# Performance work log

Measured on AMD Instinct MI355X. Metric: run time of the kernel, lower is better.

## Reference

```python
import jax, jax.numpy as jnp
import numpy as np

N, U, K, S = 1024, 64, 2, 2        # nodes, rnn_units, max_diffusion_step, num_supports
Q = S * K + 1                       # diffusion matrices (incl. identity)
B, T, H = 64, 12, 12                # batch, seq_len, horizon
IN, OUT, L = 1, 1, 2                # input_dim, output_dim, num_rnn_layers


def setup_inputs() -> dict:
    key = jax.random.key(0)
    ks = jax.random.split(key, 16)

    def glorot(k, shape):
        fan = shape[0] + shape[-1]
        return jax.random.normal(k, shape, jnp.float32) * np.float32(np.sqrt(2.0 / fan))

    # random-walk supports from a random dense adjacency (DCRNN: transpose of D^-1 A)
    adj = jax.random.uniform(ks[0], (N, N), jnp.float32)
    rw = lambda a: a / a.sum(axis=1, keepdims=True)
    supports = jnp.stack([rw(adj).T, rw(adj.T).T])  # (S, N, N)

    inputs = jax.random.normal(ks[1], (B, N * IN, T), jnp.float32)

    p = {}
    i = 2
    for pre, ind in (("enc", IN), ("dec", OUT)):
        for l in range(L):
            f = (ind if l == 0 else U) + U
            p[f"{pre}_gw{l}"] = glorot(ks[i], (Q * f, 2 * U)); i += 1
            p[f"{pre}_gb{l}"] = jnp.ones((2 * U,), jnp.float32)   # GRU gate bias init 1.0
            p[f"{pre}_cw{l}"] = glorot(ks[i], (Q * f, U)); i += 1
            p[f"{pre}_cb{l}"] = jnp.zeros((U,), jnp.float32)
    p["proj_w"] = glorot(ks[i], (U, OUT))
    p["proj_b"] = jnp.zeros((OUT,), jnp.float32)
    return {"inputs": inputs, "supports": supports, **p}


def _diffusion(x, supports):
    # x: (B, N, F) -> (B, N, Q*F); Chebyshev-style recurrence as in DCGRUCell._gconv
    mats = [x]
    for s in range(S):
        A = supports[s]
        x0 = x
        x1 = jnp.einsum('nm,bmf->bnf', A, x0)
        mats.append(x1)
        for _ in range(2, K + 1):
            x2 = 2.0 * jnp.einsum('nm,bmf->bnf', A, x1) - x0
            mats.append(x2)
            x0, x1 = x1, x2
    return jnp.concatenate(mats, axis=-1)


def _cell(x, h, supports, gw, gb, cw, cb):
    # x: (B,N,Fin), h: (B,N,U)
    ru = jax.nn.sigmoid(_diffusion(jnp.concatenate([x, h], -1), supports) @ gw + gb)
    r, u = ru[..., :U], ru[..., U:]
    c = jnp.tanh(_diffusion(jnp.concatenate([x, r * h], -1), supports) @ cw + cb)
    return u * h + (1.0 - u) * c


def reference(inputs, supports,
              enc_gw0, enc_gb0, enc_cw0, enc_cb0,
              enc_gw1, enc_gb1, enc_cw1, enc_cb1,
              dec_gw0, dec_gb0, dec_cw0, dec_cb0,
              dec_gw1, dec_gb1, dec_cw1, dec_cb1,
              proj_w, proj_b):
    enc = [(enc_gw0, enc_gb0, enc_cw0, enc_cb0), (enc_gw1, enc_gb1, enc_cw1, enc_cb1)]
    dec = [(dec_gw0, dec_gb0, dec_cw0, dec_cb0), (dec_gw1, dec_gb1, dec_cw1, dec_cb1)]

    x_seq = inputs.reshape(B, N, IN, T).transpose(3, 0, 1, 2)  # (T, B, N, IN)
    h0 = jnp.zeros((L, B, N, U), inputs.dtype)

    def enc_step(h, x):
        out, hs = x, []
        for l in range(L):
            hn = _cell(out, h[l], supports, *enc[l])
            hs.append(hn)
            out = hn
        return jnp.stack(hs), None

    hT, _ = jax.lax.scan(enc_step, h0, x_seq)

    def dec_step(carry, _):
        h, xin = carry
        out, hs = xin, []
        for l in range(L):
            hn = _cell(out, h[l], supports, *dec[l])
            hs.append(hn)
            out = hn
        proj = out @ proj_w + proj_b          # (B, N, OUT)
        return (jnp.stack(hs), proj), proj.reshape(B, N * OUT)

    go = jnp.zeros((B, N, OUT), inputs.dtype)
    _, outs = jax.lax.scan(dec_step, (hT, go), None, length=H)
    return outs  # (H, B, N*OUT)
```

## Files before the change

### kernel.cpp

```cpp
#include <hip/hip_runtime.h>

typedef _Float16 f16;
typedef _Float16 f16x4 __attribute__((ext_vector_type(4)));
typedef _Float16 f16x8 __attribute__((ext_vector_type(8)));
typedef float    f32x4 __attribute__((ext_vector_type(4)));

#define NN 1024
#define NT 12
#define NHOR 12
#define ROWS (NN*64)
#define MATH (1024*1024)
static const long SLOT = (long)NN*4096;

__device__ __forceinline__ int sw4(int row){ return (row ^ (row>>2)) & 3; }

__device__ __forceinline__ int ilvpos(int k){
  int r = k & 31;
  return (k & ~31) + ((r & 12) << 1) + (r & 3) + ((r & 16) >> 2);
}

template<int NR>
__device__ __forceinline__ void stage(f16* lds, const f16* src, int ldk, int k0, int tid){
  #pragma unroll
  for (int ic=0; ic<NR/64; ++ic){
    const int c = tid + ic*256;
    const int row = c>>2, c4 = c&3;
    const f16* g = src + (long)row*ldk + k0 + ((c4 ^ sw4(row))<<3);
    __builtin_amdgcn_global_load_lds((const __attribute__((address_space(1))) void*)g,
                                     (__attribute__((address_space(3))) void*)(lds + c*8), 16, 0, 0);
  }
}

__device__ __forceinline__ f16x8 fragI(const f16* lds, int row, int rq){
  return *(const f16x8*)&lds[row*32 + ((rq ^ sw4(row))<<3)];
}

__device__ __forceinline__ f16x8 fragN(const f16* lds, int row, int lk){
  const int s = sw4(row);
  const int cl = (lk>>3) ^ s, ch = (2|(lk>>3)) ^ s;
  f16x4 lo = *(const f16x4*)&lds[row*32 + (cl<<3) + (lk&7)];
  f16x4 hi = *(const f16x4*)&lds[row*32 + (ch<<3) + (lk&7)];
  f16x8 r; r[0]=lo[0];r[1]=lo[1];r[2]=lo[2];r[3]=lo[3];
  r[4]=hi[0];r[5]=hi[1];r[6]=hi[2];r[7]=hi[3];
  return r;
}

struct DiffP {
  const f16* W;
  const f16* Y0; const f16* Y1;
  f16* out0; f16* out1;
  int nct0;
  int mode_x;
  int wsq;
};

__global__ __launch_bounds__(256) void gemm_diff(DiffP p) {
  __shared__ f16 Ws[2][128*32];
  __shared__ f16 Ys[2][128*32];
  const int tid=threadIdx.x, l=tid&63, w=tid>>6;
  const int rq=l>>4, ro=l&15, lk=rq*4;
  const int rt=blockIdx.x, ct=blockIdx.y;
  const int part = (ct >= p.nct0);
  const int ctl  = part ? (ct - p.nct0) : ct;
  const f16* Wb = p.W + (long)rt*128*1024;
  const f16* Yb = (part ? p.Y1 : p.Y0) + (long)ctl*128*1024;
  const int wm=(w>>1)*64, wc=(w&1)*64;
  f32x4 acc[4][4] = {};
  stage<128>(Ws[0], Wb, 1024, 0, tid);
  stage<128>(Ys[0], Yb, 1024, 0, tid);
  __syncthreads();
  int cur = 0;
  for (int t=0; t<32; ++t) {
    if (t<31) {
      stage<128>(Ws[cur^1], Wb, 1024, (t+1)*32, tid);
      stage<128>(Ys[cur^1], Yb, 1024, (t+1)*32, tid);
    }
    f16x8 wf[4], yf[4];
    #pragma unroll
    for (int i=0;i<4;i++) wf[i] = fragI(Ws[cur], wm + i*16 + ro, rq);
    #pragma unroll
    for (int j=0;j<4;j++) yf[j] = fragI(Ys[cur], wc + j*16 + ro, rq);
    if (!p.wsq) {
      #pragma unroll
      for (int i=0;i<4;i++)
        #pragma unroll
        for (int j=0;j<4;j++)
          acc[i][j] = __builtin_amdgcn_mfma_f32_16x16x32_f16(wf[i], yf[j], acc[i][j], 0,0,0);
    } else {
      #pragma unroll
      for (int i=0;i<4;i++)
        #pragma unroll
        for (int j=0;j<4;j++)
          acc[i][j] = __builtin_amdgcn_mfma_f32_16x16x32_f16(yf[j], wf[i], acc[i][j], 0,0,0);
    }
    __syncthreads();
    cur ^= 1;
  }
  if (p.wsq) {
    #pragma unroll
    for (int i=0;i<4;i++){
      const long rg = (long)rt*128 + wm + i*16 + ro;
      #pragma unroll
      for (int j=0;j<4;j++){
        const int cb = ct*128 + wc + j*16 + lk;
        f16x4 sv;
        #pragma unroll
        for (int e=0;e<4;e++) sv[e] = (f16)(2.f*acc[i][j][e] - ((rg==(long)(cb+e))?1.f:0.f));
        *(f16x4*)&p.out0[rg*1024 + cb] = sv;
      }
    }
    return;
  }
  f16* ob = part ? p.out1 : p.out0;
  const int mode = part ? p.mode_x : 0;
  #pragma unroll
  for (int i=0;i<4;i++){
    #pragma unroll
    for (int e=0;e<4;e++){
      const int c = rt*128 + wm + i*16 + rq*4 + e;
      const int q = c>>10, n = c&1023;
      #pragma unroll
      for (int j=0;j<4;j++){
        const int bul = wc + j*16 + ro;
        const f16 v = (f16)acc[i][j][e];
        if (mode==0) ob[(long)q*SLOT + (long)n*4096 + (long)ctl*128 + bul] = v;
        else if (bul < 64) ob[(long)q*ROWS + n*64 + bul] = v;
      }
    }
  }
}

struct Tab5 { const f16* p[5]; };
struct CellP {
  Tab5 ta, tb, xq;
  const f16 *wa, *wb, *wx0;
  const float* bias;
  const float* h32in;
  f16* rh; f16* rhhat; float* u32;
  float* h32io; f16* h16io; f16* hhat;
  int nseg, xf1;
};

template<int O, int GATE>
__global__ __launch_bounds__(256) void cell_gemm(CellP p) {
  constexpr int FC = O/32;
  __shared__ f16 As[2][128*32];
  __shared__ f16 Bs[2][O*32];
  const int tid=threadIdx.x, l=tid&63, w=tid>>6;
  const int rq=l>>4, ro=l&15, lk=rq*4;
  const int wm=(w>>1)*64, wc=(w&1)*(O/2);
  f32x4 acc[4][FC] = {};
  const long r0 = (long)blockIdx.x*128;
  const int nt = p.nseg*10;
  auto stg = [&](int buf, int t){
    const int kg = t*32;
    const int seg = (kg>=320)?1:0;
    const int kk = kg - seg*320;
    const int q = kk>>6, kq = kk&63;
    const f16* asrc = (seg ? p.tb.p[q] : p.ta.p[q]) + r0*64;
    const f16* wsrc = seg ? p.wb : p.wa;
    stage<128>(As[buf], asrc, 64, kq, tid);
    stage<O>(Bs[buf], wsrc, 320, kk, tid);
  };
  stg(0,0);
  __syncthreads();
  int cur = 0;
  for (int t=0; t<nt; ++t) {
    if (t+1<nt) stg(cur^1, t+1);
    f16x8 a[4], b[FC];
    #pragma unroll
    for (int i=0;i<4;i++) a[i] = fragN(As[cur], wm + i*16 + ro, lk);
    #pragma unroll
    for (int j=0;j<FC;j++) b[j] = fragI(Bs[cur], wc + j*16 + ro, rq);
    #pragma unroll
    for (int i=0;i<4;i++)
      #pragma unroll
      for (int j=0;j<FC;j++)
        acc[i][j] = __builtin_amdgcn_mfma_f32_16x16x32_f16(a[i], b[j], acc[i][j], 0,0,0);
    __syncthreads();
    cur ^= 1;
  }
  #pragma unroll
  for (int i=0;i<4;i++) {
    #pragma unroll
    for (int e=0;e<4;e++) {
      const long rg = r0 + wm + i*16 + rq*4 + e;
      const int bb = (int)(rg & 63), nn2 = (int)(rg >> 6);
      const long hcol = (long)ilvpos(nn2);
      float xv[5];
      if (p.xf1) {
        #pragma unroll
        for (int q2=0;q2<5;q2++) xv[q2] = (float)p.xq.p[q2][rg];
      }
      #pragma unroll
      for (int j=0;j<FC;j++) {
        const int col = wc + j*16 + ro;
        float v = acc[i][j][e] + p.bias[col];
        if (p.xf1) {
          #pragma unroll
          for (int q2=0;q2<5;q2++) v += xv[q2] * (float)p.wx0[q2*O + col];
        }
        if (GATE) {
          const float s = 1.f/(1.f + __expf(-v));
          if (col < 64) {
            const float rhv = s * p.h32in[rg*64 + col];
            p.rh[rg*64 + col] = (f16)rhv;
            p.rhhat[((long)bb*64 + col)*1024 + hcol] = (f16)rhv;
          } else {
            p.u32[rg*64 + (col-64)] = s;
          }
        } else {
          const float cc = tanhf(v);
          const float u  = p.u32[rg*64 + col];
          const float h  = p.h32io[rg*64 + col];
          const float hn = u*h + (1.f-u)*cc;
          p.h32io[rg*64 + col] = hn;
          p.h16io[rg*64 + col] = (f16)hn;
          p.hhat[((long)bb*64 + col)*1024 + hcol] = (f16)hn;
        }
      }
    }
  }
}

__global__ __launch_bounds__(256) void k_transpose(const f16* in, f16* out, int R, int C) {
  __shared__ f16 T[64*66];
  const long rb = (long)blockIdx.x*64, cb = (long)blockIdx.y*64;
  const int t = threadIdx.x;
  #pragma unroll
  for (int it=0; it<2; ++it) {
    const int r = (t>>3) + it*32, c8 = (t&7)*8;
    f16x8 v = *(const f16x8*)(in + (rb+r)*C + cb + c8);
    *(f16x8*)&T[r*66 + c8] = v;
  }
  __syncthreads();
  #pragma unroll
  for (int it=0; it<2; ++it) {
    const int c = (t>>3) + it*32, r8 = (t&7)*8;
    f16x8 v;
    #pragma unroll
    for (int j=0;j<8;j++) v[j] = T[(r8+j)*66 + c];
    *(f16x8*)(out + (cb+c)*R + rb + r8) = v;
  }
}

__global__ void k_cast_sup(const float* s, f16* o) {
  long i = (long)blockIdx.x*256 + threadIdx.x;
  if (i < 2LL*MATH) o[i] = (f16)s[i];
}

__global__ void k_ilv(const f16* in, f16* out) {
  int i = blockIdx.x*256 + threadIdx.x;
  if (i >= MATH) return;
  int r = i>>10, k = i&1023;
  out[(long)r*1024 + ilvpos(k)] = in[i];
}

__global__ void k_pack_x(const float* in, f16* xe, f16* xet) {
  int i = blockIdx.x*256 + threadIdx.x;
  if (i >= NT*ROWS) return;
  int t = i / ROWS, r = i % ROWS, n = r>>6, b = r&63;
  float v = in[(long)b*NN*NT + (long)n*NT + t];
  xe[i] = (f16)v;
  xet[(long)t*131072 + (long)b*1024 + ilvpos(n)] = (f16)v;
}

__global__ void k_split_w_t(const float* src, f16* wh_t, f16* wxA, int f, int xf, int O) {
  int i = blockIdx.x*256 + threadIdx.x;
  if (i >= 5*f*O) return;
  int o = i % O, rr = i / O, q = rr / f, ff = rr % f;
  f16 v = (f16)src[i];
  if (ff < xf) {
    if (xf == 1) wxA[q*O + o] = v;
    else         wxA[(long)o*320 + q*64 + ilvpos(ff)] = v;
  } else {
    wh_t[(long)o*320 + q*64 + ilvpos(ff - xf)] = v;
  }
}

__global__ void k_proj(const float* h32, const float* pw, const float* pb,
                       float* out, f16* xdec, f16* xdect) {
  int r = blockIdx.x*256 + threadIdx.x;
  if (r >= ROWS) return;
  float acc = pb[0];
  const float* hp = h32 + (long)r*64;
  #pragma unroll
  for (int k=0;k<64;k++) acc += hp[k]*pw[k];
  int n = r>>6, b = r&63;
  out[(long)b*NN + n] = acc;
  xdec[r] = (f16)acc;
  xdect[(long)b*1024 + ilvpos(n)] = (f16)acc;
}

extern "C" void kernel_launch(void* const* d_in, const int* in_sizes, int n_in,
                              void* d_out, int out_size, void* d_ws, size_t ws_size,
                              hipStream_t stream) {
  (void)in_sizes; (void)n_in; (void)out_size; (void)ws_size;
  const float* inputs = (const float*)d_in[0];
  const float* sup    = (const float*)d_in[1];
  const float* gwp[4] = {(const float*)d_in[2], (const float*)d_in[6], (const float*)d_in[10], (const float*)d_in[14]};
  const float* gbp[4] = {(const float*)d_in[3], (const float*)d_in[7], (const float*)d_in[11], (const float*)d_in[15]};
  const float* cwp[4] = {(const float*)d_in[4], (const float*)d_in[8], (const float*)d_in[12], (const float*)d_in[16]};
  const float* cbp[4] = {(const float*)d_in[5], (const float*)d_in[9], (const float*)d_in[13], (const float*)d_in[17]};
  const float* pw = (const float*)d_in[18];
  const float* pb = (const float*)d_in[19];
  float* out = (float*)d_out;

  char* base = (char*)d_ws; size_t off = 0;
  auto alloc = [&](size_t bytes)->void* { void* p = base + off; off += (bytes + 255) & ~(size_t)255; return p; };
  f16* W16int = (f16*)alloc(4LL*MATH*2);
  f16* xenc   = (f16*)alloc((long)NT*ROWS*2);
  f16* xet    = (f16*)alloc((long)NT*131072*2);
  f16* xdec   = (f16*)alloc((long)ROWS*2);
  f16* xdect  = (f16*)alloc(131072L*2);
  f16*  h16[2]  = {(f16*)alloc((long)ROWS*64*2),  (f16*)alloc((long)ROWS*64*2)};
  f16*  hh[2]   = {(f16*)alloc(4096L*1024*2),     (f16*)alloc(4096L*1024*2)};
  float* h32[2] = {(float*)alloc((long)ROWS*64*4), (float*)alloc((long)ROWS*64*4)};
  float* u32 = (float*)alloc((long)ROWS*64*4);
  f16* rh    = (f16*)alloc((long)ROWS*64*2);
  f16* rhh   = (f16*)alloc(4096L*1024*2);
  f16* Dh    = (f16*)alloc(4*SLOT*2);
  f16* Dx    = (f16*)alloc(4*SLOT*2);
  f16* Dx0   = (f16*)alloc(4LL*ROWS*2);
  f16 *gwh[4], *gwx[4], *cwh[4], *cwx[4];
  for (int i=0;i<4;i++) {
    gwh[i]=(f16*)alloc(128L*320*2); gwx[i]=(f16*)alloc(128L*320*2);
    cwh[i]=(f16*)alloc(64L*320*2);  cwx[i]=(f16*)alloc(64L*320*2);
  }

  hipMemsetAsync(h16[0], 0, (long)ROWS*64*2, stream);
  hipMemsetAsync(h16[1], 0, (long)ROWS*64*2, stream);
  hipMemsetAsync(hh[0],  0, 4096L*1024*2, stream);
  hipMemsetAsync(hh[1],  0, 4096L*1024*2, stream);
  hipMemsetAsync(h32[0], 0, (long)ROWS*64*4, stream);
  hipMemsetAsync(h32[1], 0, (long)ROWS*64*4, stream);
  hipMemsetAsync(xdec,   0, (long)ROWS*2, stream);
  hipMemsetAsync(xdect,  0, 131072L*2, stream);

  f16* tmpA   = Dh;
  f16* tmpAt  = Dh + 2L*MATH;
  f16* tmpAti = Dh + 4L*MATH;
  f16* tmpSq  = Dh + 5L*MATH;
  k_cast_sup<<<(2*MATH+255)/256, 256, 0, stream>>>(sup, tmpA);
  for (int s=0;s<2;s++) {
    k_transpose<<<dim3(16,16),256,0,stream>>>(tmpA + (long)s*MATH, tmpAt + (long)s*MATH, 1024, 1024);
    k_ilv<<<4096,256,0,stream>>>(tmpA + (long)s*MATH, W16int + (long)(2*s)*MATH);
  }
  for (int s=0;s<2;s++) {
    k_ilv<<<4096,256,0,stream>>>(tmpAt + (long)s*MATH, tmpAti);
    DiffP mp{};
    mp.W = W16int + (long)(2*s)*MATH; mp.Y0 = tmpAti; mp.Y1 = tmpAti;
    mp.out0 = tmpSq; mp.nct0 = 8; mp.wsq = 1;
    gemm_diff<<<dim3(8,8),256,0,stream>>>(mp);
    k_ilv<<<4096,256,0,stream>>>(tmpSq, W16int + (long)(2*s+1)*MATH);
  }
  k_pack_x<<<(NT*ROWS+255)/256,256,0,stream>>>(inputs, xenc, xet);
  const int fs[4]  = {65,128,65,128};
  const int xfs[4] = {1,64,1,64};
  for (int i=0;i<4;i++) {
    k_split_w_t<<<(5*fs[i]*128+255)/256,256,0,stream>>>(gwp[i], gwh[i], gwx[i], fs[i], xfs[i], 128);
    k_split_w_t<<<(5*fs[i]*64 +255)/256,256,0,stream>>>(cwp[i], cwh[i], cwx[i], fs[i], xfs[i], 64);
  }

  auto run_cell = [&](const f16* xraw, const f16* xhat, int xf,
                      f16* h16c, f16* hhatc, float* h32c, int wi) {
    DiffP dp{};
    dp.W = W16int; dp.Y0 = hhatc; dp.out0 = Dh; dp.nct0 = 32; dp.wsq = 0;
    int gy;
    if (xf == 64) { dp.Y1 = xhat; dp.out1 = Dx;  dp.mode_x = 0; gy = 64; }
    else          { dp.Y1 = xhat; dp.out1 = Dx0; dp.mode_x = 2; gy = 33; }
    gemm_diff<<<dim3(32, gy), 256, 0, stream>>>(dp);
    CellP gp{};
    gp.ta.p[0] = h16c; for (int q=1;q<5;q++) gp.ta.p[q] = Dh + (long)(q-1)*SLOT;
    gp.wa = gwh[wi]; gp.bias = gbp[wi];
    gp.h32in = h32c; gp.rh = rh; gp.rhhat = rhh; gp.u32 = u32;
    if (xf == 64) {
      gp.nseg = 2; gp.xf1 = 0;
      gp.tb.p[0] = xraw; for (int q=1;q<5;q++) gp.tb.p[q] = Dx + (long)(q-1)*SLOT;
      gp.wb = gwx[wi];
    } else {
      gp.nseg = 1; gp.xf1 = 1;
      gp.xq.p[0] = xraw; for (int q=1;q<5;q++) gp.xq.p[q] = Dx0 + (long)(q-1)*ROWS;
      gp.wx0 = gwx[wi];
    }
    cell_gemm<128,1><<<512, 256, 0, stream>>>(gp);
    DiffP dp2{};
    dp2.W = W16int; dp2.Y0 = rhh; dp2.Y1 = rhh; dp2.out0 = Dh; dp2.nct0 = 32; dp2.wsq = 0;
    gemm_diff<<<dim3(32, 32), 256, 0, stream>>>(dp2);
    CellP cp{};
    cp.ta.p[0] = rh; for (int q=1;q<5;q++) cp.ta.p[q] = Dh + (long)(q-1)*SLOT;
    cp.wa = cwh[wi]; cp.bias = cbp[wi];
    cp.u32 = u32; cp.h32io = h32c; cp.h16io = h16c; cp.hhat = hhatc;
    if (xf == 64) {
      cp.nseg = 2; cp.xf1 = 0;
      cp.tb.p[0] = xraw; for (int q=1;q<5;q++) cp.tb.p[q] = Dx + (long)(q-1)*SLOT;
      cp.wb = cwx[wi];
    } else {
      cp.nseg = 1; cp.xf1 = 1;
      cp.xq.p[0] = xraw; for (int q=1;q<5;q++) cp.xq.p[q] = Dx0 + (long)(q-1)*ROWS;
      cp.wx0 = cwx[wi];
    }
    cell_gemm<64,0><<<512, 256, 0, stream>>>(cp);
  };

  for (int t=0;t<NT;t++) {
    run_cell(xenc + (long)t*ROWS, xet + (long)t*131072, 1, h16[0], hh[0], h32[0], 0);
    run_cell(h16[0], hh[0],                            64, h16[1], hh[1], h32[1], 1);
  }
  for (int s=0;s<NHOR;s++) {
    run_cell(xdec,   xdect,   1, h16[0], hh[0], h32[0], 2);
    run_cell(h16[0], hh[0],  64, h16[1], hh[1], h32[1], 3);
    k_proj<<<ROWS/256, 256, 0, stream>>>(h32[1], pw, pb, out + (long)s*ROWS, xdec, xdect);
  }
}
```

Before: 12.61 ms.

## Enlarge diffusion GEMM tiles to 256x256 with 4-stage LDS pipeline and XCD remap

Rewrites gemm_diff to use 512-thread workgroups computing 256x256 output tiles, each wave holding 128x64. It uses a 4-deep LDS ring with two stages of prefetch, explicit vmcnt/lgkmcnt waits, raw barriers and setprio around the MFMA block. A block-index remap spreads consecutive workgroups across XCDs for cache locality. The x-hat buffers are padded to 256 columns and zeroed so the larger tiles read valid data, and grids are shrunk to match. Separately, cell_gemm drops its double buffering in favour of a single-buffered loop, which may expose load latency there.

```diff
diff --git a/kernel.cpp b/kernel.cpp
--- a/kernel.cpp
+++ b/kernel.cpp
@@ -19,6 +19,11 @@
   return (k & ~31) + ((r & 12) << 1) + (r & 3) + ((r & 16) >> 2);
 }
 
+__device__ __forceinline__ void gld(const f16* g, f16* l){
+  __builtin_amdgcn_global_load_lds((const __attribute__((address_space(1))) void*)g,
+                                   (__attribute__((address_space(3))) void*)l, 16, 0, 0);
+}
+
 template<int NR>
 __device__ __forceinline__ void stage(f16* lds, const f16* src, int ldk, int k0, int tid){
   #pragma unroll
@@ -26,15 +31,12 @@
     const int c = tid + ic*256;
     const int row = c>>2, c4 = c&3;
     const f16* g = src + (long)row*ldk + k0 + ((c4 ^ sw4(row))<<3);
-    __builtin_amdgcn_global_load_lds((const __attribute__((address_space(1))) void*)g,
-                                     (__attribute__((address_space(3))) void*)(lds + c*8), 16, 0, 0);
-  }
-}
-
+    gld(g, lds + c*8);
+  }
+}
 __device__ __forceinline__ f16x8 fragI(const f16* lds, int row, int rq){
   return *(const f16x8*)&lds[row*32 + ((rq ^ sw4(row))<<3)];
 }
-
 __device__ __forceinline__ f16x8 fragN(const f16* lds, int row, int lk){
   const int s = sw4(row);
   const int cl = (lk>>3) ^ s, ch = (2|(lk>>3)) ^ s;
@@ -46,67 +48,81 @@
 }
 
 struct DiffP {
-  const f16* W;
-  const f16* Y0; const f16* Y1;
+  const f16* W; const f16* Y0; const f16* Y1;
   f16* out0; f16* out1;
-  int nct0;
-  int mode_x;
-  int wsq;
+  int nct0; int mode_x; int wsq;
 };
 
-__global__ __launch_bounds__(256) void gemm_diff(DiffP p) {
-  __shared__ f16 Ws[2][128*32];
-  __shared__ f16 Ys[2][128*32];
+__global__ __launch_bounds__(512, 2) void gemm_diff(DiffP p) {
+  __shared__ f16 L[4][16384];
   const int tid=threadIdx.x, l=tid&63, w=tid>>6;
-  const int rq=l>>4, ro=l&15, lk=rq*4;
-  const int rt=blockIdx.x, ct=blockIdx.y;
-  const int part = (ct >= p.nct0);
-  const int ctl  = part ? (ct - p.nct0) : ct;
-  const f16* Wb = p.W + (long)rt*128*1024;
-  const f16* Yb = (part ? p.Y1 : p.Y0) + (long)ctl*128*1024;
-  const int wm=(w>>1)*64, wc=(w&1)*64;
-  f32x4 acc[4][4] = {};
-  stage<128>(Ws[0], Wb, 1024, 0, tid);
-  stage<128>(Ys[0], Yb, 1024, 0, tid);
-  __syncthreads();
-  int cur = 0;
+  const int ro=l&15, rq=l>>4;
+  const int gx = gridDim.x;
+  int lin = blockIdx.y*gx + blockIdx.x;
+  const int nwg = gx*gridDim.y;
+  lin = (lin & 7)*(nwg>>3) + (lin>>3);
+  const int rt = lin % gx, ct = lin / gx;
+  const int part = (ct >= p.nct0) ? 1 : 0;
+  const int ctl  = part ? ct - p.nct0 : ct;
+  const f16* Wb = p.W + (long)rt*(256*1024);
+  const f16* Yb = (part ? p.Y1 : p.Y0) + (long)ctl*(256*1024);
+  const int wm=(w>>2)*128, wc=(w&3)*64;
+  const int ca=tid, cb2=tid+512;
+  const int ra=ca>>2, pa=ca&3, rb=cb2>>2, pb2=cb2&3;
+  const long sa = (long)ra*1024 + ((pa ^ (ra&3))<<3);
+  const long sb = (long)rb*1024 + ((pb2 ^ (rb&3))<<3);
+  const int da = ra*32 + pa*8, db = rb*32 + pb2*8;
+  f32x4 acc[8][4] = {};
+  auto STAGE = [&](int tt){
+    f16* Lr = L[tt&3]; const int k0 = tt*32;
+    gld(Wb+k0+sa, Lr+da);      gld(Wb+k0+sb, Lr+db);
+    gld(Yb+k0+sa, Lr+8192+da); gld(Yb+k0+sb, Lr+8192+db);
+  };
+  STAGE(0); STAGE(1);
+  asm volatile("s_waitcnt vmcnt(4)" ::: "memory");
+  __builtin_amdgcn_s_barrier();
   for (int t=0; t<32; ++t) {
-    if (t<31) {
-      stage<128>(Ws[cur^1], Wb, 1024, (t+1)*32, tid);
-      stage<128>(Ys[cur^1], Yb, 1024, (t+1)*32, tid);
-    }
-    f16x8 wf[4], yf[4];
-    #pragma unroll
-    for (int i=0;i<4;i++) wf[i] = fragI(Ws[cur], wm + i*16 + ro, rq);
-    #pragma unroll
-    for (int j=0;j<4;j++) yf[j] = fragI(Ys[cur], wc + j*16 + ro, rq);
+    const f16* Lw = L[t&3];
+    const f16* Ly = Lw + 8192;
+    f16x8 wf[8], yf[4];
+    #pragma unroll
+    for (int i=0;i<8;i++){ const int r=wm+i*16+ro; wf[i]=*(const f16x8*)&Lw[r*32+((rq^(r&3))<<3)]; }
+    #pragma unroll
+    for (int j=0;j<4;j++){ const int r=wc+j*16+ro; yf[j]=*(const f16x8*)&Ly[r*32+((rq^(r&3))<<3)]; }
+    if (t+2 < 32) STAGE(t+2);
+    asm volatile("s_waitcnt lgkmcnt(0)" ::: "memory");
+    __builtin_amdgcn_sched_barrier(0);
+    __builtin_amdgcn_s_setprio(1);
     if (!p.wsq) {
       #pragma unroll
-      for (int i=0;i<4;i++)
+      for (int i=0;i<8;i++)
         #pragma unroll
         for (int j=0;j<4;j++)
-          acc[i][j] = __builtin_amdgcn_mfma_f32_16x16x32_f16(wf[i], yf[j], acc[i][j], 0,0,0);
+          acc[i][j]=__builtin_amdgcn_mfma_f32_16x16x32_f16(wf[i],yf[j],acc[i][j],0,0,0);
     } else {
       #pragma unroll
-      for (int i=0;i<4;i++)
+      for (int i=0;i<8;i++)
         #pragma unroll
         for (int j=0;j<4;j++)
-          acc[i][j] = __builtin_amdgcn_mfma_f32_16x16x32_f16(yf[j], wf[i], acc[i][j], 0,0,0);
-    }
-    __syncthreads();
-    cur ^= 1;
+          acc[i][j]=__builtin_amdgcn_mfma_f32_16x16x32_f16(yf[j],wf[i],acc[i][j],0,0,0);
+    }
+    __builtin_amdgcn_s_setprio(0);
+    if (t==31) break;
+    if (t<29) { asm volatile("s_waitcnt vmcnt(4)" ::: "memory"); }
+    else      { asm volatile("s_waitcnt vmcnt(0)" ::: "memory"); }
+    __builtin_amdgcn_s_barrier();
   }
   if (p.wsq) {
     #pragma unroll
-    for (int i=0;i<4;i++){
-      const long rg = (long)rt*128 + wm + i*16 + ro;
+    for (int i=0;i<8;i++){
+      const int n = rt*256 + wm + i*16 + ro;
       #pragma unroll
       for (int j=0;j<4;j++){
-        const int cb = ct*128 + wc + j*16 + lk;
+        const int m0 = ct*256 + wc + j*16 + rq*4;
         f16x4 sv;
         #pragma unroll
-        for (int e=0;e<4;e++) sv[e] = (f16)(2.f*acc[i][j][e] - ((rg==(long)(cb+e))?1.f:0.f));
-        *(f16x4*)&p.out0[rg*1024 + cb] = sv;
+        for (int e=0;e<4;e++) sv[e] = (f16)(2.f*acc[i][j][e] - ((n==m0+e)?1.f:0.f));
+        *(f16x4*)&p.out0[(long)n*1024 + m0] = sv;
       }
     }
     return;
@@ -114,17 +130,20 @@
   f16* ob = part ? p.out1 : p.out0;
   const int mode = part ? p.mode_x : 0;
   #pragma unroll
-  for (int i=0;i<4;i++){
+  for (int i=0;i<8;i++){
     #pragma unroll
     for (int e=0;e<4;e++){
-      const int c = rt*128 + wm + i*16 + rq*4 + e;
-      const int q = c>>10, n = c&1023;
+      const int c = rt*256 + wm + i*16 + rq*4 + e;
+      const int q = c>>10, nn = c&1023;
       #pragma unroll
       for (int j=0;j<4;j++){
-        const int bul = wc + j*16 + ro;
         const f16 v = (f16)acc[i][j][e];
-        if (mode==0) ob[(long)q*SLOT + (long)n*4096 + (long)ctl*128 + bul] = v;
-        else if (bul < 64) ob[(long)q*ROWS + n*64 + bul] = v;
+        if (mode==0) {
+          ob[(long)q*SLOT + (long)nn*4096 + (long)ctl*256 + wc + j*16 + ro] = v;
+        } else {
+          const int bul = wc + j*16 + ro;
+          if (bul < 64) ob[(long)q*ROWS + nn*64 + bul] = v;
+        }
       }
     }
   }
@@ -144,41 +163,34 @@
 template<int O, int GATE>
 __global__ __launch_bounds__(256) void cell_gemm(CellP p) {
   constexpr int FC = O/32;
-  __shared__ f16 As[2][128*32];
-  __shared__ f16 Bs[2][O*32];
+  __shared__ f16 As[128*32];
+  __shared__ f16 Bs[O*32];
   const int tid=threadIdx.x, l=tid&63, w=tid>>6;
   const int rq=l>>4, ro=l&15, lk=rq*4;
   const int wm=(w>>1)*64, wc=(w&1)*(O/2);
   f32x4 acc[4][FC] = {};
   const long r0 = (long)blockIdx.x*128;
-  const int nt = p.nseg*10;
-  auto stg = [&](int buf, int t){
-    const int kg = t*32;
-    const int seg = (kg>=320)?1:0;
-    const int kk = kg - seg*320;
+  const int Ktot = p.nseg*320;
+  for (int kg=0; kg<Ktot; kg+=32) {
+    const int seg = (kg>=320) ? 1 : 0;
+    const int kk  = kg - seg*320;
     const int q = kk>>6, kq = kk&63;
     const f16* asrc = (seg ? p.tb.p[q] : p.ta.p[q]) + r0*64;
     const f16* wsrc = seg ? p.wb : p.wa;
-    stage<128>(As[buf], asrc, 64, kq, tid);
-    stage<O>(Bs[buf], wsrc, 320, kk, tid);
-  };
-  stg(0,0);
-  __syncthreads();
-  int cur = 0;
-  for (int t=0; t<nt; ++t) {
-    if (t+1<nt) stg(cur^1, t+1);
+    stage<128>(As, asrc, 64, kq, tid);
+    stage<O>(Bs, wsrc, 320, kk, tid);
+    __syncthreads();
     f16x8 a[4], b[FC];
     #pragma unroll
-    for (int i=0;i<4;i++) a[i] = fragN(As[cur], wm + i*16 + ro, lk);
-    #pragma unroll
-    for (int j=0;j<FC;j++) b[j] = fragI(Bs[cur], wc + j*16 + ro, rq);
+    for (int i=0;i<4;i++) a[i] = fragN(As, wm + i*16 + ro, lk);
+    #pragma unroll
+    for (int j=0;j<FC;j++) b[j] = fragI(Bs, wc + j*16 + ro, rq);
     #pragma unroll
     for (int i=0;i<4;i++)
       #pragma unroll
       for (int j=0;j<FC;j++)
         acc[i][j] = __builtin_amdgcn_mfma_f32_16x16x32_f16(a[i], b[j], acc[i][j], 0,0,0);
     __syncthreads();
-    cur ^= 1;
   }
   #pragma unroll
   for (int i=0;i<4;i++) {
@@ -262,7 +274,7 @@
   int t = i / ROWS, r = i % ROWS, n = r>>6, b = r&63;
   float v = in[(long)b*NN*NT + (long)n*NT + t];
   xe[i] = (f16)v;
-  xet[(long)t*131072 + (long)b*1024 + ilvpos(n)] = (f16)v;
+  xet[(long)t*262144 + (long)b*1024 + ilvpos(n)] = (f16)v;
 }
 
 __global__ void k_split_w_t(const float* src, f16* wh_t, f16* wxA, int f, int xf, int O) {
@@ -310,9 +322,9 @@
   auto alloc = [&](size_t bytes)->void* { void* p = base + off; off += (bytes + 255) & ~(size_t)255; return p; };
   f16* W16int = (f16*)alloc(4LL*MATH*2);
   f16* xenc   = (f16*)alloc((long)NT*ROWS*2);
-  f16* xet    = (f16*)alloc((long)NT*131072*2);
+  f16* xet    = (f16*)alloc((long)NT*262144*2);
   f16* xdec   = (f16*)alloc((long)ROWS*2);
-  f16* xdect  = (f16*)alloc(131072L*2);
+  f16* xdect  = (f16*)alloc(262144L*2);
   f16*  h16[2]  = {(f16*)alloc((long)ROWS*64*2),  (f16*)alloc((long)ROWS*64*2)};
   f16*  hh[2]   = {(f16*)alloc(4096L*1024*2),     (f16*)alloc(4096L*1024*2)};
   float* h32[2] = {(float*)alloc((long)ROWS*64*4), (float*)alloc((long)ROWS*64*4)};
@@ -335,7 +347,8 @@
   hipMemsetAsync(h32[0], 0, (long)ROWS*64*4, stream);
   hipMemsetAsync(h32[1], 0, (long)ROWS*64*4, stream);
   hipMemsetAsync(xdec,   0, (long)ROWS*2, stream);
-  hipMemsetAsync(xdect,  0, 131072L*2, stream);
+  hipMemsetAsync(xdect,  0, 262144L*2, stream);
+  hipMemsetAsync(xet,    0, (long)NT*262144*2, stream);
 
   f16* tmpA   = Dh;
   f16* tmpAt  = Dh + 2L*MATH;
@@ -350,8 +363,8 @@
     k_ilv<<<4096,256,0,stream>>>(tmpAt + (long)s*MATH, tmpAti);
     DiffP mp{};
     mp.W = W16int + (long)(2*s)*MATH; mp.Y0 = tmpAti; mp.Y1 = tmpAti;
-    mp.out0 = tmpSq; mp.nct0 = 8; mp.wsq = 1;
-    gemm_diff<<<dim3(8,8),256,0,stream>>>(mp);
+    mp.out0 = tmpSq; mp.nct0 = 4; mp.wsq = 1;
+    gemm_diff<<<dim3(4,4),512,0,stream>>>(mp);
     k_ilv<<<4096,256,0,stream>>>(tmpSq, W16int + (long)(2*s+1)*MATH);
   }
   k_pack_x<<<(NT*ROWS+255)/256,256,0,stream>>>(inputs, xenc, xet);
@@ -365,11 +378,11 @@
   auto run_cell = [&](const f16* xraw, const f16* xhat, int xf,
                       f16* h16c, f16* hhatc, float* h32c, int wi) {
     DiffP dp{};
-    dp.W = W16int; dp.Y0 = hhatc; dp.out0 = Dh; dp.nct0 = 32; dp.wsq = 0;
+    dp.W = W16int; dp.Y0 = hhatc; dp.out0 = Dh; dp.nct0 = 16; dp.wsq = 0;
     int gy;
-    if (xf == 64) { dp.Y1 = xhat; dp.out1 = Dx;  dp.mode_x = 0; gy = 64; }
-    else          { dp.Y1 = xhat; dp.out1 = Dx0; dp.mode_x = 2; gy = 33; }
-    gemm_diff<<<dim3(32, gy), 256, 0, stream>>>(dp);
+    if (xf == 64) { dp.Y1 = xhat; dp.out1 = Dx;  dp.mode_x = 0; gy = 32; }
+    else          { dp.Y1 = xhat; dp.out1 = Dx0; dp.mode_x = 2; gy = 17; }
+    gemm_diff<<<dim3(16, gy), 512, 0, stream>>>(dp);
     CellP gp{};
     gp.ta.p[0] = h16c; for (int q=1;q<5;q++) gp.ta.p[q] = Dh + (long)(q-1)*SLOT;
     gp.wa = gwh[wi]; gp.bias = gbp[wi];
@@ -385,8 +398,8 @@
     }
     cell_gemm<128,1><<<512, 256, 0, stream>>>(gp);
     DiffP dp2{};
-    dp2.W = W16int; dp2.Y0 = rhh; dp2.Y1 = rhh; dp2.out0 = Dh; dp2.nct0 = 32; dp2.wsq = 0;
-    gemm_diff<<<dim3(32, 32), 256, 0, stream>>>(dp2);
+    dp2.W = W16int; dp2.Y0 = rhh; dp2.Y1 = rhh; dp2.out0 = Dh; dp2.nct0 = 16; dp2.wsq = 0;
+    gemm_diff<<<dim3(16, 16), 512, 0, stream>>>(dp2);
     CellP cp{};
     cp.ta.p[0] = rh; for (int q=1;q<5;q++) cp.ta.p[q] = Dh + (long)(q-1)*SLOT;
     cp.wa = cwh[wi]; cp.bias = cbp[wi];
@@ -404,7 +417,7 @@
   };
 
   for (int t=0;t<NT;t++) {
-    run_cell(xenc + (long)t*ROWS, xet + (long)t*131072, 1, h16[0], hh[0], h32[0], 0);
+    run_cell(xenc + (long)t*ROWS, xet + (long)t*262144, 1, h16[0], hh[0], h32[0], 0);
     run_cell(h16[0], hh[0],                            64, h16[1], hh[1], h32[1], 1);
   }
   for (int s=0;s<NHOR;s++) {
```

After: 43.89 ms. +248.0%, slower.
